# Kernel optimization log

Hardware: AMD Instinct MI355X
Metric: run time of the kernel (lower is better)

Reference implementation:

```python
import jax, jax.numpy as jnp
import numpy as np

N = 20000      # nodes
E = 320000     # edges (avg degree 16)
F_IN = 768
DIMS = [(768, 1536), (1536, 768), (768, 384), (384, 256), (256, 5)]


def setup_inputs() -> dict:
    key = jax.random.key(0)
    ks = jax.random.split(key, 2 + 3 * len(DIMS))
    inp = {
        'x': jax.random.normal(ks[0], (N, F_IN), dtype=jnp.float32),
        'edge_index': jax.random.randint(ks[1], (2, E), 0, N, dtype=jnp.int64),
    }
    for li, (fi, fo) in enumerate(DIMS):
        s = 1.0 / np.sqrt(fi)
        inp[f'Wl{li+1}'] = jax.random.uniform(ks[2 + 3 * li], (fi, fo), jnp.float32, -s, s)
        inp[f'Wr{li+1}'] = jax.random.uniform(ks[3 + 3 * li], (fi, fo), jnp.float32, -s, s)
        inp[f'b{li+1}'] = jax.random.uniform(ks[4 + 3 * li], (fo,), jnp.float32, -s, s)
    return inp


def _sage_conv(x, src, dst, deg_inv, Wl, Wr, b):
    # mean aggregate neighbor features, then linear (mean commutes with linear,
    # matching PyG SAGEConv which aggregates x_j then applies lin_l)
    agg = jax.ops.segment_sum(x[src], dst, num_segments=N) * deg_inv  # [N, F_in]
    return agg @ Wl + x @ Wr + b


def reference(x, edge_index,
              Wl1, Wr1, b1, Wl2, Wr2, b2, Wl3, Wr3, b3,
              Wl4, Wr4, b4, Wl5, Wr5, b5):
    src, dst = edge_index[0], edge_index[1]
    deg = jax.ops.segment_sum(jnp.ones((E,), jnp.float32), dst, num_segments=N)
    deg_inv = (1.0 / jnp.maximum(deg, 1.0))[:, None]  # clamp like PyG mean aggr

    h = jax.nn.relu(_sage_conv(x, src, dst, deg_inv, Wl1, Wr1, b1))
    h = jax.nn.relu(_sage_conv(h, src, dst, deg_inv, Wl2, Wr2, b2))
    h = jax.nn.relu(_sage_conv(h, src, dst, deg_inv, Wl3, Wr3, b3))
    h = jax.nn.relu(_sage_conv(h, src, dst, deg_inv, Wl4, Wr4, b4))  # [N, 256]
    out = _sage_conv(h, src, dst, deg_inv, Wl5, Wr5, b5)             # [N, 5]
    return (h, out)
```

## Files before the change

### kernel.cpp

```cpp
#include <hip/hip_runtime.h>
#include <stdint.h>

typedef __attribute__((ext_vector_type(8))) short short8;
typedef __attribute__((ext_vector_type(4))) float f32x4;

__device__ __forceinline__ float bf2f(unsigned short s) {
  return __uint_as_float(((unsigned)s) << 16);
}
__device__ __forceinline__ unsigned short f2bf(float f) {
  unsigned u = __float_as_uint(f);
  u += 0x7fffu + ((u >> 16) & 1u);
  return (unsigned short)(u >> 16);
}

__global__ void gs_count_deg(const int* __restrict__ dst, int* __restrict__ cnt, int E) {
  int e = blockIdx.x * 256 + threadIdx.x;
  if (e < E) atomicAdd(&cnt[dst[e]], 1);
}

__global__ void gs_scanA(const int* __restrict__ cnt, int* __restrict__ rp,
                         int* __restrict__ bsum, int n) {
  __shared__ int sm[256];
  const int b = blockIdx.x, t = threadIdx.x;
  const int base = b * 1024 + t * 4;
  int v[4]; int s = 0;
#pragma unroll
  for (int i = 0; i < 4; ++i) { v[i] = (base + i < n) ? cnt[base + i] : 0; s += v[i]; }
  sm[t] = s;
  __syncthreads();
  for (int off = 1; off < 256; off <<= 1) {
    int x = (t >= off) ? sm[t - off] : 0;
    __syncthreads();
    sm[t] += x;
    __syncthreads();
  }
  int run = sm[t] - s;
#pragma unroll
  for (int i = 0; i < 4; ++i) { if (base + i < n) rp[base + i] = run; run += v[i]; }
  if (t == 255) bsum[b] = sm[255];
}

__global__ void gs_scanB(int* bsum, int nb) {
  if (threadIdx.x == 0 && blockIdx.x == 0) {
    int run = 0;
    for (int i = 0; i < nb; ++i) { int v = bsum[i]; bsum[i] = run; run += v; }
    bsum[nb] = run;
  }
}

__global__ void gs_scanC(int* __restrict__ rp, int* __restrict__ cur,
                         const int* __restrict__ bsum, int n, int nb) {
  int i = blockIdx.x * 256 + threadIdx.x;
  if (i < n) {
    int v = rp[i] + bsum[i >> 10];
    rp[i] = v;
    cur[i] = v;
  }
  if (i == n) rp[n] = bsum[nb];
}

__global__ void gs_fill_csr(const int* __restrict__ src, const int* __restrict__ dst,
                            int* __restrict__ cur, int* __restrict__ col, int E) {
  int e = blockIdx.x * 256 + threadIdx.x;
  if (e < E) {
    int pos = atomicAdd(&cur[dst[e]], 1);
    col[pos] = src[e];
  }
}

__global__ void gs_f32_to_bf16(const float* __restrict__ in, unsigned short* __restrict__ out, int n4) {
  int i = blockIdx.x * 256 + threadIdx.x;
  if (i < n4) {
    float4 f = ((const float4*)in)[i];
    ushort4 o;
    o.x = f2bf(f.x); o.y = f2bf(f.y); o.z = f2bf(f.z); o.w = f2bf(f.w);
    ((ushort4*)out)[i] = o;
  }
}

struct TP { const float* W; unsigned short* WT; int K, F; };
struct TP8 { TP t[8]; };

__global__ void gs_tpack8(TP8 args) {
  const TP a = args.t[blockIdx.z];
  const int k0 = blockIdx.x * 32, f0 = blockIdx.y * 32;
  if (k0 >= a.K || f0 >= a.F) return;
  __shared__ float t[32][33];
  const int tx = threadIdx.x, ty = threadIdx.y;
#pragma unroll
  for (int r = ty; r < 32; r += 8) {
    int k = k0 + r, f = f0 + tx;
    t[r][tx] = (k < a.K && f < a.F) ? a.W[(size_t)k * a.F + f] : 0.f;
  }
  __syncthreads();
#pragma unroll
  for (int r = ty; r < 32; r += 8) {
    int f = f0 + r, k = k0 + tx;
    if (f < a.F && k < a.K) a.WT[(size_t)f * a.K + k] = f2bf(t[tx][r]);
  }
}

__global__ __launch_bounds__(64)
void gs_agg_slice(const unsigned short* __restrict__ C, int ldc, int zoff,
                  const int* __restrict__ rp, const int* __restrict__ col,
                  const float* __restrict__ bias,
                  unsigned short* __restrict__ hout, float* __restrict__ fout,
                  int F, int relu) {
  const int v = blockIdx.x;
  const int cc = blockIdx.y * 128 + 2 * threadIdx.x;
  const int l = threadIdx.x;
  const int s0 = rp[v], s1 = rp[v + 1];
  const float inv = 1.0f / (float)max(s1 - s0, 1);
  float a0 = 0.f, a1 = 0.f;
  __shared__ int nb[64];
  for (int base = s0; base < s1; base += 64) {
    int m = min(s1 - base, 64);
    __syncthreads();
    if (l < m) nb[l] = col[base + l];
    __syncthreads();
    int j = 0;
    for (; j + 4 <= m; j += 4) {
      ushort2 u0 = *(const ushort2*)(C + (size_t)nb[j + 0] * ldc + cc);
      ushort2 u1 = *(const ushort2*)(C + (size_t)nb[j + 1] * ldc + cc);
      ushort2 u2 = *(const ushort2*)(C + (size_t)nb[j + 2] * ldc + cc);
      ushort2 u3 = *(const ushort2*)(C + (size_t)nb[j + 3] * ldc + cc);
      a0 += bf2f(u0.x) + bf2f(u1.x) + bf2f(u2.x) + bf2f(u3.x);
      a1 += bf2f(u0.y) + bf2f(u1.y) + bf2f(u2.y) + bf2f(u3.y);
    }
    for (; j < m; ++j) {
      ushort2 u = *(const ushort2*)(C + (size_t)nb[j] * ldc + cc);
      a0 += bf2f(u.x); a1 += bf2f(u.y);
    }
  }
  float o0 = a0 * inv, o1 = a1 * inv;
  if (zoff >= 0) {
    ushort2 u = *(const ushort2*)(C + (size_t)v * ldc + zoff + cc);
    o0 += bf2f(u.x); o1 += bf2f(u.y);
  }
  if (bias) { o0 += bias[cc]; o1 += bias[cc + 1]; }
  if (relu) { o0 = fmaxf(o0, 0.f); o1 = fmaxf(o1, 0.f); }
  if (hout) {
    ushort2 u; u.x = f2bf(o0); u.y = f2bf(o1);
    *(ushort2*)(hout + (size_t)v * F + cc) = u;
  }
  if (fout) *(float2*)(fout + (size_t)v * F + cc) = make_float2(o0, o1);
}

__global__ __launch_bounds__(256)
void gs_gemm(const unsigned short* __restrict__ A1, const unsigned short* __restrict__ A2,
             const unsigned short* __restrict__ B1, const unsigned short* __restrict__ B2,
             const float* __restrict__ bias, unsigned short* __restrict__ Hout,
             int M, int Nn, int K, int doRelu, int Mt, int Nt) {
  __shared__ unsigned short lA[128 * 64];
  __shared__ unsigned short lB[128 * 64];
  const int tid = threadIdx.x;
  const int wid = tid >> 6;
  const int lane = tid & 63;

  const int MG = 8;
  const int per = MG * Nt;
  const int g = blockIdx.x / per;
  const int rem = blockIdx.x - g * per;
  const int gsz = min(MG, Mt - g * MG);
  const int nIdx = rem / gsz;
  const int mIdx = g * MG + (rem - nIdx * gsz);
  const int bM = mIdx * 128;
  const int bN = nIdx * 128;
  const int wM = (wid >> 1) * 64;
  const int wN = (wid & 1) * 64;

  f32x4 acc[4][4];
#pragma unroll
  for (int i = 0; i < 4; ++i)
#pragma unroll
    for (int j = 0; j < 4; ++j) acc[i][j] = (f32x4){0.f, 0.f, 0.f, 0.f};

  const int mrow = wM + (lane & 15);
  const int nrow = wN + (lane & 15);
  const int q = lane >> 4;
  const int swz = lane & 7;
  const int srow = wid * 8 + (lane >> 3);
  const int sc = (lane & 7) ^ (lane >> 3);
  const int npass = A2 ? 2 : 1;

  for (int pass = 0; pass < npass; ++pass) {
    const unsigned short* Ap = pass ? A2 : A1;
    const unsigned short* Bp = pass ? B2 : B1;
    for (int k0 = 0; k0 < K; k0 += 64) {
#pragma unroll
      for (int r = 0; r < 4; ++r) {
        int row = r * 32 + srow;
        int ga = bM + row;
        if (ga >= M) ga = M - 1;
        const unsigned short* gpA = Ap + (size_t)ga * K + k0 + sc * 8;
        const unsigned short* gpB = Bp + (size_t)(bN + row) * K + k0 + sc * 8;
        unsigned lo = (unsigned)(r * 32 + wid * 8) * 128;
        __builtin_amdgcn_global_load_lds(
            (const __attribute__((address_space(1))) unsigned int*)gpA,
            (__attribute__((address_space(3))) unsigned int*)((char*)lA + lo), 16, 0, 0);
        __builtin_amdgcn_global_load_lds(
            (const __attribute__((address_space(1))) unsigned int*)gpB,
            (__attribute__((address_space(3))) unsigned int*)((char*)lB + lo), 16, 0, 0);
      }
      __syncthreads();
#pragma unroll
      for (int s = 0; s < 2; ++s) {
        const int cofs = ((s * 4 + q) ^ swz) * 8;
        short8 aF[4], bF[4];
#pragma unroll
        for (int i = 0; i < 4; ++i) {
          aF[i] = *(const short8*)&lA[(mrow + i * 16) * 64 + cofs];
          bF[i] = *(const short8*)&lB[(nrow + i * 16) * 64 + cofs];
        }
#pragma unroll
        for (int i = 0; i < 4; ++i)
#pragma unroll
          for (int j = 0; j < 4; ++j)
            acc[i][j] = __builtin_amdgcn_mfma_f32_16x16x32_bf16(aF[i], bF[j], acc[i][j], 0, 0, 0);
      }
      __syncthreads();
    }
  }

  const int rbase = bM + wM + (lane >> 4) * 4;
#pragma unroll
  for (int i = 0; i < 4; ++i) {
#pragma unroll
    for (int r = 0; r < 4; ++r) {
      int row = rbase + i * 16 + r;
      if (row >= M) continue;
#pragma unroll
      for (int j = 0; j < 4; ++j) {
        int colN = bN + wN + j * 16 + (lane & 15);
        float v = acc[i][j][r];
        if (bias) v += bias[colN];
        if (doRelu) v = fmaxf(v, 0.f);
        Hout[(size_t)row * Nn + colN] = f2bf(v);
      }
    }
  }
}

__global__ __launch_bounds__(64)
void gs_l5dot(const unsigned short* __restrict__ h4, const float* __restrict__ Wl,
              const float* __restrict__ Wr, float* __restrict__ yz) {
  __shared__ float sW[2560];
  const int v = blockIdx.x;
  const int l = threadIdx.x;
  for (int i = l; i < 2560; i += 64) sW[i] = (i < 1280) ? Wl[i] : Wr[i - 1280];
  __syncthreads();
  ushort4 u = ((const ushort4*)(h4 + (size_t)v * 256))[l];
  float hv[4] = {bf2f(u.x), bf2f(u.y), bf2f(u.z), bf2f(u.w)};
  float acc[10];
#pragma unroll
  for (int n = 0; n < 10; ++n) acc[n] = 0.f;
#pragma unroll
  for (int t = 0; t < 4; ++t) {
    int k = 4 * l + t;
#pragma unroll
    for (int n = 0; n < 5; ++n) {
      acc[n] += hv[t] * sW[k * 5 + n];
      acc[5 + n] += hv[t] * sW[1280 + k * 5 + n];
    }
  }
#pragma unroll
  for (int n = 0; n < 10; ++n)
    for (int off = 32; off > 0; off >>= 1) acc[n] += __shfl_down(acc[n], off, 64);
  if (l == 0) {
#pragma unroll
    for (int n = 0; n < 10; ++n) yz[(size_t)v * 10 + n] = acc[n];
  }
}

__global__ __launch_bounds__(64)
void gs_l5agg(const float* __restrict__ yz, const int* __restrict__ rp,
              const int* __restrict__ col, const float* __restrict__ b,
              float* __restrict__ out) {
  const int v = blockIdx.x;
  const int l = threadIdx.x;
  const int s0 = rp[v], s1 = rp[v + 1];
  const float inv = 1.0f / (float)max(s1 - s0, 1);
  float acc[5] = {0.f, 0.f, 0.f, 0.f, 0.f};
  for (int e = s0 + l; e < s1; e += 64) {
    const float* yr = yz + (size_t)col[e] * 10;
#pragma unroll
    for (int n = 0; n < 5; ++n) acc[n] += yr[n];
  }
#pragma unroll
  for (int n = 0; n < 5; ++n)
    for (int off = 32; off > 0; off >>= 1) acc[n] += __shfl_down(acc[n], off, 64);
  if (l == 0) {
#pragma unroll
    for (int n = 0; n < 5; ++n)
      out[(size_t)v * 5 + n] = acc[n] * inv + yz[(size_t)v * 10 + 5 + n] + b[n];
  }
}

extern "C" void kernel_launch(void* const* d_in, const int* in_sizes, int n_in,
                              void* d_out, int out_size, void* d_ws, size_t ws_size,
                              hipStream_t stream) {
  const float* x = (const float*)d_in[0];
  const int* ei = (const int*)d_in[1];
  const int N = in_sizes[0] / 768;
  const int E = in_sizes[1] / 2;
  const int* src = ei;
  const int* dst = ei + E;

  const float* Wl[5];
  const float* Wr[5];
  const float* bb[5];
  for (int l = 0; l < 5; ++l) {
    Wl[l] = (const float*)d_in[2 + 3 * l];
    Wr[l] = (const float*)d_in[3 + 3 * l];
    bb[l] = (const float*)d_in[4 + 3 * l];
  }

  char* w = (char*)d_ws;
  size_t off = 0;
  auto take = [&](size_t bytes) -> char* {
    char* p = w + off;
    off = (off + bytes + 255) & ~(size_t)255;
    return p;
  };
  unsigned short* ar1 = (unsigned short*)take((size_t)N * 768 * 2);
  unsigned short* ar2 = (unsigned short*)take((size_t)N * 768 * 2);
  unsigned short* ar3 = (unsigned short*)take((size_t)N * 1536 * 2);
  unsigned short* C2  = (unsigned short*)take((size_t)N * 1536 * 2);
  int* cnt  = (int*)take((size_t)N * 4);
  int* rp   = (int*)take((size_t)(N + 1) * 4);
  int* cur  = (int*)take((size_t)N * 4);
  int* col  = (int*)take((size_t)E * 4);
  const int nbChunks = (N + 1023) / 1024;
  int* bsum = (int*)take((size_t)(nbChunks + 1) * 4);
  unsigned short* WT1l = (unsigned short*)take((size_t)1536 * 768 * 2);
  unsigned short* WT1r = (unsigned short*)take((size_t)1536 * 768 * 2);
  unsigned short* WT2  = (unsigned short*)take((size_t)1536 * 1536 * 2);
  unsigned short* WT3  = (unsigned short*)take((size_t)768 * 768 * 2);
  unsigned short* WT4  = (unsigned short*)take((size_t)512 * 384 * 2);

  unsigned short* xb   = ar1;
  unsigned short* C3   = ar1;
  unsigned short* aggb = ar2;
  unsigned short* h2   = ar2;
  unsigned short* h1   = ar3;
  unsigned short* C4   = ar3;
  unsigned short* h3   = ar3 + (size_t)N * 512;
  unsigned short* h4   = ar3 + (size_t)N * (512 + 384);
  float*          yz5  = (float*)(ar3 + (size_t)N * (512 + 384 + 256));

  const int M = N;
  const int Mt = (M + 127) / 128;

  hipMemsetAsync(cnt, 0, (size_t)N * 4, stream);
  gs_count_deg<<<(E + 255) / 256, 256, 0, stream>>>(dst, cnt, E);
  gs_scanA<<<nbChunks, 256, 0, stream>>>(cnt, rp, bsum, N);
  gs_scanB<<<1, 64, 0, stream>>>(bsum, nbChunks);
  gs_scanC<<<(N + 256) / 256, 256, 0, stream>>>(rp, cur, bsum, N, nbChunks);
  gs_fill_csr<<<(E + 255) / 256, 256, 0, stream>>>(src, dst, cur, col, E);

  gs_f32_to_bf16<<<((N * 768 / 4) + 255) / 256, 256, 0, stream>>>(x, xb, N * 768 / 4);
  TP8 tp;
  tp.t[0] = {Wl[0], WT1l, 768, 1536};
  tp.t[1] = {Wr[0], WT1r, 768, 1536};
  tp.t[2] = {Wl[1], WT2, 1536, 768};
  tp.t[3] = {Wr[1], WT2 + (size_t)768 * 1536, 1536, 768};
  tp.t[4] = {Wl[2], WT3, 768, 384};
  tp.t[5] = {Wr[2], WT3 + (size_t)384 * 768, 768, 384};
  tp.t[6] = {Wl[3], WT4, 384, 256};
  tp.t[7] = {Wr[3], WT4 + (size_t)256 * 384, 384, 256};
  gs_tpack8<<<dim3(48, 48, 8), dim3(32, 8), 0, stream>>>(tp);

  float* houtF = (float*)d_out;
  float* out5  = (float*)d_out + (size_t)N * 256;

  gs_agg_slice<<<dim3(N, 6), 64, 0, stream>>>(xb, 768, -1, rp, col, nullptr, aggb, nullptr, 768, 0);
  gs_gemm<<<Mt * 12, 256, 0, stream>>>(aggb, xb, WT1l, WT1r, bb[0], h1, M, 1536, 768, 1, Mt, 12);

  gs_gemm<<<Mt * 12, 256, 0, stream>>>(h1, nullptr, WT2, nullptr, nullptr, C2, M, 1536, 1536, 0, Mt, 12);
  gs_agg_slice<<<dim3(N, 6), 64, 0, stream>>>(C2, 1536, 768, rp, col, bb[1], h2, nullptr, 768, 1);

  gs_gemm<<<Mt * 6, 256, 0, stream>>>(h2, nullptr, WT3, nullptr, nullptr, C3, M, 768, 768, 0, Mt, 6);
  gs_agg_slice<<<dim3(N, 3), 64, 0, stream>>>(C3, 768, 384, rp, col, bb[2], h3, nullptr, 384, 1);

  gs_gemm<<<Mt * 4, 256, 0, stream>>>(h3, nullptr, WT4, nullptr, nullptr, C4, M, 512, 384, 0, Mt, 4);
  gs_agg_slice<<<dim3(N, 2), 64, 0, stream>>>(C4, 512, 256, rp, col, bb[3], h4, houtF, 256, 1);

  gs_l5dot<<<N, 64, 0, stream>>>(h4, Wl[4], Wr[4], yz5);
  gs_l5agg<<<N, 64, 0, stream>>>(yz5, rp, col, bb[4], out5);
}
```

Before: 687.1 us.

## Restructure neighbor aggregation: 64-col slices, 4 edges per wave in parallel

Replaces the per-node 128-column aggregation kernel with a wave-per-(slice,node) kernel. Each wave covers 64 columns, with 16 lanes each loading 4 bf16 values and 4 lane groups processing different edges at once, reduced by cross-lane shuffles. Neighbor indices are passed by shuffle instead of shared memory plus two barriers. Blocks now pack 4 waves. The aim is more memory-level parallelism and wider loads on the gather. The cost is masked tail work and a shuffle reduction, and only a quarter of lanes do the epilogue.

```diff
diff --git a/kernel.cpp b/kernel.cpp
--- a/kernel.cpp
+++ b/kernel.cpp
@@ -100,50 +100,66 @@
   }
 }
 
-__global__ __launch_bounds__(64)
-void gs_agg_slice(const unsigned short* __restrict__ C, int ldc, int zoff,
-                  const int* __restrict__ rp, const int* __restrict__ col,
-                  const float* __restrict__ bias,
-                  unsigned short* __restrict__ hout, float* __restrict__ fout,
-                  int F, int relu) {
-  const int v = blockIdx.x;
-  const int cc = blockIdx.y * 128 + 2 * threadIdx.x;
-  const int l = threadIdx.x;
+__global__ __launch_bounds__(256)
+void gs_agg_w4(const unsigned short* __restrict__ C, int ldc, int zoff,
+               const int* __restrict__ rp, const int* __restrict__ col,
+               const float* __restrict__ bias,
+               unsigned short* __restrict__ hout, float* __restrict__ fout,
+               int F, int N, int relu) {
+  const int S = F >> 6;
+  const int idx = blockIdx.x * 4 + (threadIdx.x >> 6);
+  if (idx >= N * S) return;
+  const int s = idx / N;
+  const int v = idx - s * N;
+  const int lane = threadIdx.x & 63;
+  const int slot = lane >> 4;
+  const int l16 = lane & 15;
+  const int cc = s * 64 + l16 * 4;
   const int s0 = rp[v], s1 = rp[v + 1];
   const float inv = 1.0f / (float)max(s1 - s0, 1);
-  float a0 = 0.f, a1 = 0.f;
-  __shared__ int nb[64];
+  float a0 = 0.f, a1 = 0.f, a2 = 0.f, a3 = 0.f;
+
   for (int base = s0; base < s1; base += 64) {
-    int m = min(s1 - base, 64);
-    __syncthreads();
-    if (l < m) nb[l] = col[base + l];
-    __syncthreads();
-    int j = 0;
-    for (; j + 4 <= m; j += 4) {
-      ushort2 u0 = *(const ushort2*)(C + (size_t)nb[j + 0] * ldc + cc);
-      ushort2 u1 = *(const ushort2*)(C + (size_t)nb[j + 1] * ldc + cc);
-      ushort2 u2 = *(const ushort2*)(C + (size_t)nb[j + 2] * ldc + cc);
-      ushort2 u3 = *(const ushort2*)(C + (size_t)nb[j + 3] * ldc + cc);
-      a0 += bf2f(u0.x) + bf2f(u1.x) + bf2f(u2.x) + bf2f(u3.x);
-      a1 += bf2f(u0.y) + bf2f(u1.y) + bf2f(u2.y) + bf2f(u3.y);
+    const int m = min(s1 - base, 64);
+    const int nbv = col[base + min(lane, m - 1)];
+    const int iters = (m + 3) >> 2;
+    for (int it = 0; it < iters; it += 4) {
+#pragma unroll
+      for (int u = 0; u < 4; ++u) {
+        int e = (it + u) * 4 + slot;
+        int row = __shfl(nbv, min(e, m - 1), 64);
+        ushort4 x = *(const ushort4*)(C + (size_t)row * ldc + cc);
+        float w = (e < m) ? 1.f : 0.f;
+        a0 += w * bf2f(x.x); a1 += w * bf2f(x.y);
+        a2 += w * bf2f(x.z); a3 += w * bf2f(x.w);
+      }
     }
-    for (; j < m; ++j) {
-      ushort2 u = *(const ushort2*)(C + (size_t)nb[j] * ldc + cc);
-      a0 += bf2f(u.x); a1 += bf2f(u.y);
-    }
-  }
-  float o0 = a0 * inv, o1 = a1 * inv;
+  }
+  a0 += __shfl_xor(a0, 16, 64); a1 += __shfl_xor(a1, 16, 64);
+  a2 += __shfl_xor(a2, 16, 64); a3 += __shfl_xor(a3, 16, 64);
+  a0 += __shfl_xor(a0, 32, 64); a1 += __shfl_xor(a1, 32, 64);
+  a2 += __shfl_xor(a2, 32, 64); a3 += __shfl_xor(a3, 32, 64);
+  if (slot != 0) return;
+
+  float o0 = a0 * inv, o1 = a1 * inv, o2 = a2 * inv, o3 = a3 * inv;
   if (zoff >= 0) {
-    ushort2 u = *(const ushort2*)(C + (size_t)v * ldc + zoff + cc);
-    o0 += bf2f(u.x); o1 += bf2f(u.y);
-  }
-  if (bias) { o0 += bias[cc]; o1 += bias[cc + 1]; }
-  if (relu) { o0 = fmaxf(o0, 0.f); o1 = fmaxf(o1, 0.f); }
+    ushort4 u = *(const ushort4*)(C + (size_t)v * ldc + zoff + cc);
+    o0 += bf2f(u.x); o1 += bf2f(u.y); o2 += bf2f(u.z); o3 += bf2f(u.w);
+  }
+  if (bias) {
+    float4 b = *(const float4*)(bias + cc);
+    o0 += b.x; o1 += b.y; o2 += b.z; o3 += b.w;
+  }
+  if (relu) {
+    o0 = fmaxf(o0, 0.f); o1 = fmaxf(o1, 0.f);
+    o2 = fmaxf(o2, 0.f); o3 = fmaxf(o3, 0.f);
+  }
   if (hout) {
-    ushort2 u; u.x = f2bf(o0); u.y = f2bf(o1);
-    *(ushort2*)(hout + (size_t)v * F + cc) = u;
-  }
-  if (fout) *(float2*)(fout + (size_t)v * F + cc) = make_float2(o0, o1);
+    ushort4 u;
+    u.x = f2bf(o0); u.y = f2bf(o1); u.z = f2bf(o2); u.w = f2bf(o3);
+    *(ushort4*)(hout + (size_t)v * F + cc) = u;
+  }
+  if (fout) *(float4*)(fout + (size_t)v * F + cc) = make_float4(o0, o1, o2, o3);
 }
 
 __global__ __launch_bounds__(256)
@@ -373,17 +389,17 @@
   float* houtF = (float*)d_out;
   float* out5  = (float*)d_out + (size_t)N * 256;
 
-  gs_agg_slice<<<dim3(N, 6), 64, 0, stream>>>(xb, 768, -1, rp, col, nullptr, aggb, nullptr, 768, 0);
+  gs_agg_w4<<<(N * 12 + 3) / 4, 256, 0, stream>>>(xb, 768, -1, rp, col, nullptr, aggb, nullptr, 768, N, 0);
   gs_gemm<<<Mt * 12, 256, 0, stream>>>(aggb, xb, WT1l, WT1r, bb[0], h1, M, 1536, 768, 1, Mt, 12);
 
   gs_gemm<<<Mt * 12, 256, 0, stream>>>(h1, nullptr, WT2, nullptr, nullptr, C2, M, 1536, 1536, 0, Mt, 12);
-  gs_agg_slice<<<dim3(N, 6), 64, 0, stream>>>(C2, 1536, 768, rp, col, bb[1], h2, nullptr, 768, 1);
+  gs_agg_w4<<<(N * 12 + 3) / 4, 256, 0, stream>>>(C2, 1536, 768, rp, col, bb[1], h2, nullptr, 768, N, 1);
 
   gs_gemm<<<Mt * 6, 256, 0, stream>>>(h2, nullptr, WT3, nullptr, nullptr, C3, M, 768, 768, 0, Mt, 6);
-  gs_agg_slice<<<dim3(N, 3), 64, 0, stream>>>(C3, 768, 384, rp, col, bb[2], h3, nullptr, 384, 1);
+  gs_agg_w4<<<(N * 6 + 3) / 4, 256, 0, stream>>>(C3, 768, 384, rp, col, bb[2], h3, nullptr, 384, N, 1);
 
   gs_gemm<<<Mt * 4, 256, 0, stream>>>(h3, nullptr, WT4, nullptr, nullptr, C4, M, 512, 384, 0, Mt, 4);
-  gs_agg_slice<<<dim3(N, 2), 64, 0, stream>>>(C4, 512, 256, rp, col, bb[3], h4, houtF, 256, 1);
+  gs_agg_w4<<<(N * 4 + 3) / 4, 256, 0, stream>>>(C4, 512, 256, rp, col, bb[3], h4, houtF, 256, N, 1);
 
   gs_l5dot<<<N, 64, 0, stream>>>(h4, Wl[4], Wr[4], yz5);
   gs_l5agg<<<N, 64, 0, stream>>>(yz5, rp, col, bb[4], out5);
```

After: 807.4 us. 17.5% more time.

## Split neighbor gather across wave halves with zero-row padding; batch layer-5 dot rows

Applied to the files above, without the earlier changes.

The aggregation kernel now covers 64 columns per block. The two 32-lane halves of the wave gather alternating neighbors, with 8 independent loads in flight each, and their sums are combined with a cross-half shuffle. Neighbor lists are padded to a multiple of 16 with a dedicated zero row appended to each gathered matrix, which removes the remainder loop. This needs a small zeroing kernel and a reshuffled workspace layout. Separately, the layer-5 dot kernel processes 8 nodes per block so the 10 KB weight staging into shared memory is amortized. The padding adds wasted loads on low-degree nodes, and the grid doubles to twice as many blocks.

```diff
diff --git a/kernel.cpp b/kernel.cpp
--- a/kernel.cpp
+++ b/kernel.cpp
@@ -78,6 +78,15 @@
   }
 }
 
+__global__ void gs_zero3(unsigned short* __restrict__ a, int na,
+                         unsigned short* __restrict__ b, int nb,
+                         unsigned short* __restrict__ c, int nc) {
+  int i = blockIdx.x * 256 + threadIdx.x;
+  if (i < na) a[i] = 0;
+  if (i < nb) b[i] = 0;
+  if (i < nc) c[i] = 0;
+}
+
 struct TP { const float* W; unsigned short* WT; int K, F; };
 struct TP8 { TP t[8]; };
 
@@ -101,43 +110,49 @@
 }
 
 __global__ __launch_bounds__(64)
-void gs_agg_slice(const unsigned short* __restrict__ C, int ldc, int zoff,
-                  const int* __restrict__ rp, const int* __restrict__ col,
-                  const float* __restrict__ bias,
-                  unsigned short* __restrict__ hout, float* __restrict__ fout,
-                  int F, int relu) {
+void gs_agg64(const unsigned short* __restrict__ C, int ldc, int zoff,
+              const int* __restrict__ rp, const int* __restrict__ col,
+              const float* __restrict__ bias,
+              unsigned short* __restrict__ hout, float* __restrict__ fout,
+              int F, int zrow, int relu) {
   const int v = blockIdx.x;
-  const int cc = blockIdx.y * 128 + 2 * threadIdx.x;
-  const int l = threadIdx.x;
+  const int lane = threadIdx.x;
+  const int half = lane >> 5;
+  const int cc = blockIdx.y * 64 + (lane & 31) * 2;
   const int s0 = rp[v], s1 = rp[v + 1];
   const float inv = 1.0f / (float)max(s1 - s0, 1);
   float a0 = 0.f, a1 = 0.f;
+
   __shared__ int nb[64];
   for (int base = s0; base < s1; base += 64) {
-    int m = min(s1 - base, 64);
+    const int m = min(s1 - base, 64);
+    const int mp = (m + 15) & ~15;
     __syncthreads();
-    if (l < m) nb[l] = col[base + l];
+    if (lane < m) nb[lane] = col[base + lane];
+    else if (lane < mp) nb[lane] = zrow;
     __syncthreads();
-    int j = 0;
-    for (; j + 4 <= m; j += 4) {
-      ushort2 u0 = *(const ushort2*)(C + (size_t)nb[j + 0] * ldc + cc);
-      ushort2 u1 = *(const ushort2*)(C + (size_t)nb[j + 1] * ldc + cc);
-      ushort2 u2 = *(const ushort2*)(C + (size_t)nb[j + 2] * ldc + cc);
-      ushort2 u3 = *(const ushort2*)(C + (size_t)nb[j + 3] * ldc + cc);
-      a0 += bf2f(u0.x) + bf2f(u1.x) + bf2f(u2.x) + bf2f(u3.x);
-      a1 += bf2f(u0.y) + bf2f(u1.y) + bf2f(u2.y) + bf2f(u3.y);
+    for (int j = 0; j < mp; j += 16) {
+      ushort2 u[8];
+#pragma unroll
+      for (int t = 0; t < 8; ++t)
+        u[t] = *(const ushort2*)(C + (size_t)nb[j + 2 * t + half] * ldc + cc);
+#pragma unroll
+      for (int t = 0; t < 8; ++t) { a0 += bf2f(u[t].x); a1 += bf2f(u[t].y); }
     }
-    for (; j < m; ++j) {
-      ushort2 u = *(const ushort2*)(C + (size_t)nb[j] * ldc + cc);
-      a0 += bf2f(u.x); a1 += bf2f(u.y);
-    }
-  }
+  }
+  a0 += __shfl_xor(a0, 32, 64);
+  a1 += __shfl_xor(a1, 32, 64);
+  if (half) return;
+
   float o0 = a0 * inv, o1 = a1 * inv;
   if (zoff >= 0) {
     ushort2 u = *(const ushort2*)(C + (size_t)v * ldc + zoff + cc);
     o0 += bf2f(u.x); o1 += bf2f(u.y);
   }
-  if (bias) { o0 += bias[cc]; o1 += bias[cc + 1]; }
+  if (bias) {
+    float2 b = *(const float2*)(bias + cc);
+    o0 += b.x; o1 += b.y;
+  }
   if (relu) { o0 = fmaxf(o0, 0.f); o1 = fmaxf(o1, 0.f); }
   if (hout) {
     ushort2 u; u.x = f2bf(o0); u.y = f2bf(o1);
@@ -243,32 +258,36 @@
 
 __global__ __launch_bounds__(64)
 void gs_l5dot(const unsigned short* __restrict__ h4, const float* __restrict__ Wl,
-              const float* __restrict__ Wr, float* __restrict__ yz) {
+              const float* __restrict__ Wr, float* __restrict__ yz, int N) {
   __shared__ float sW[2560];
-  const int v = blockIdx.x;
   const int l = threadIdx.x;
   for (int i = l; i < 2560; i += 64) sW[i] = (i < 1280) ? Wl[i] : Wr[i - 1280];
   __syncthreads();
-  ushort4 u = ((const ushort4*)(h4 + (size_t)v * 256))[l];
-  float hv[4] = {bf2f(u.x), bf2f(u.y), bf2f(u.z), bf2f(u.w)};
-  float acc[10];
-#pragma unroll
-  for (int n = 0; n < 10; ++n) acc[n] = 0.f;
-#pragma unroll
-  for (int t = 0; t < 4; ++t) {
-    int k = 4 * l + t;
-#pragma unroll
-    for (int n = 0; n < 5; ++n) {
-      acc[n] += hv[t] * sW[k * 5 + n];
-      acc[5 + n] += hv[t] * sW[1280 + k * 5 + n];
+  const int v0 = blockIdx.x * 8;
+  for (int vi = 0; vi < 8; ++vi) {
+    const int v = v0 + vi;
+    if (v >= N) return;
+    ushort4 u = ((const ushort4*)(h4 + (size_t)v * 256))[l];
+    float hv[4] = {bf2f(u.x), bf2f(u.y), bf2f(u.z), bf2f(u.w)};
+    float acc[10];
+#pragma unroll
+    for (int n = 0; n < 10; ++n) acc[n] = 0.f;
+#pragma unroll
+    for (int t = 0; t < 4; ++t) {
+      int k = 4 * l + t;
+#pragma unroll
+      for (int n = 0; n < 5; ++n) {
+        acc[n] += hv[t] * sW[k * 5 + n];
+        acc[5 + n] += hv[t] * sW[1280 + k * 5 + n];
+      }
     }
-  }
-#pragma unroll
-  for (int n = 0; n < 10; ++n)
-    for (int off = 32; off > 0; off >>= 1) acc[n] += __shfl_down(acc[n], off, 64);
-  if (l == 0) {
-#pragma unroll
-    for (int n = 0; n < 10; ++n) yz[(size_t)v * 10 + n] = acc[n];
+#pragma unroll
+    for (int n = 0; n < 10; ++n)
+      for (int off = 32; off > 0; off >>= 1) acc[n] += __shfl_down(acc[n], off, 64);
+    if (l == 0) {
+#pragma unroll
+      for (int n = 0; n < 10; ++n) yz[(size_t)v * 10 + n] = acc[n];
+    }
   }
 }
 
@@ -322,10 +341,11 @@
     off = (off + bytes + 255) & ~(size_t)255;
     return p;
   };
-  unsigned short* ar1 = (unsigned short*)take((size_t)N * 768 * 2);
+  unsigned short* ar1 = (unsigned short*)take((size_t)(N + 1) * 768 * 2);
   unsigned short* ar2 = (unsigned short*)take((size_t)N * 768 * 2);
   unsigned short* ar3 = (unsigned short*)take((size_t)N * 1536 * 2);
-  unsigned short* C2  = (unsigned short*)take((size_t)N * 1536 * 2);
+  unsigned short* C2  = (unsigned short*)take((size_t)(N + 1) * 1536 * 2);
+  unsigned short* C4  = (unsigned short*)take((size_t)(N + 1) * 512 * 2);
   int* cnt  = (int*)take((size_t)N * 4);
   int* rp   = (int*)take((size_t)(N + 1) * 4);
   int* cur  = (int*)take((size_t)N * 4);
@@ -343,10 +363,9 @@
   unsigned short* aggb = ar2;
   unsigned short* h2   = ar2;
   unsigned short* h1   = ar3;
-  unsigned short* C4   = ar3;
-  unsigned short* h3   = ar3 + (size_t)N * 512;
-  unsigned short* h4   = ar3 + (size_t)N * (512 + 384);
-  float*          yz5  = (float*)(ar3 + (size_t)N * (512 + 384 + 256));
+  unsigned short* h3   = ar3;
+  unsigned short* h4   = ar3 + (size_t)N * 384;
+  float*          yz5  = (float*)(ar3 + (size_t)N * (384 + 256));
 
   const int M = N;
   const int Mt = (M + 127) / 128;
@@ -359,6 +378,9 @@
   gs_fill_csr<<<(E + 255) / 256, 256, 0, stream>>>(src, dst, cur, col, E);
 
   gs_f32_to_bf16<<<((N * 768 / 4) + 255) / 256, 256, 0, stream>>>(x, xb, N * 768 / 4);
+  gs_zero3<<<6, 256, 0, stream>>>(xb + (size_t)N * 768, 768,
+                                  C2 + (size_t)N * 1536, 1536,
+                                  C4 + (size_t)N * 512, 512);
   TP8 tp;
   tp.t[0] = {Wl[0], WT1l, 768, 1536};
   tp.t[1] = {Wr[0], WT1r, 768, 1536};
@@ -373,18 +395,18 @@
   float* houtF = (float*)d_out;
   float* out5  = (float*)d_out + (size_t)N * 256;
 
-  gs_agg_slice<<<dim3(N, 6), 64, 0, stream>>>(xb, 768, -1, rp, col, nullptr, aggb, nullptr, 768, 0);
+  gs_agg64<<<dim3(N, 12), 64, 0, stream>>>(xb, 768, -1, rp, col, nullptr, aggb, nullptr, 768, N, 0);
   gs_gemm<<<Mt * 12, 256, 0, stream>>>(aggb, xb, WT1l, WT1r, bb[0], h1, M, 1536, 768, 1, Mt, 12);
 
   gs_gemm<<<Mt * 12, 256, 0, stream>>>(h1, nullptr, WT2, nullptr, nullptr, C2, M, 1536, 1536, 0, Mt, 12);
-  gs_agg_slice<<<dim3(N, 6), 64, 0, stream>>>(C2, 1536, 768, rp, col, bb[1], h2, nullptr, 768, 1);
+  gs_agg64<<<dim3(N, 12), 64, 0, stream>>>(C2, 1536, 768, rp, col, bb[1], h2, nullptr, 768, N, 1);
 
   gs_gemm<<<Mt * 6, 256, 0, stream>>>(h2, nullptr, WT3, nullptr, nullptr, C3, M, 768, 768, 0, Mt, 6);
-  gs_agg_slice<<<dim3(N, 3), 64, 0, stream>>>(C3, 768, 384, rp, col, bb[2], h3, nullptr, 384, 1);
+  gs_agg64<<<dim3(N, 6), 64, 0, stream>>>(C3, 768, 384, rp, col, bb[2], h3, nullptr, 384, N, 1);
 
   gs_gemm<<<Mt * 4, 256, 0, stream>>>(h3, nullptr, WT4, nullptr, nullptr, C4, M, 512, 384, 0, Mt, 4);
-  gs_agg_slice<<<dim3(N, 2), 64, 0, stream>>>(C4, 512, 256, rp, col, bb[3], h4, houtF, 256, 1);
-
-  gs_l5dot<<<N, 64, 0, stream>>>(h4, Wl[4], Wr[4], yz5);
+  gs_agg64<<<dim3(N, 4), 64, 0, stream>>>(C4, 512, 256, rp, col, bb[3], h4, houtF, 256, N, 1);
+
+  gs_l5dot<<<(N + 7) / 8, 64, 0, stream>>>(h4, Wl[4], Wr[4], yz5, N);
   gs_l5agg<<<N, 64, 0, stream>>>(yz5, rp, col, bb[4], out5);
 }
```

After: 705.1 us. 1.03x slower.
